# Kernel optimization log

Hardware: AMD Instinct MI355X
Metric: run time of the kernel (lower is better)

The kernel has to match this reference:

```python
import jax, jax.numpy as jnp
import numpy as np

TAU = 2.0        # tau_m
EPS = 1e-5       # BatchNorm eps
SG_GAIN = 4.0    # surrogate gradient gain for LIF nodes
GATE_GAIN = 10.0 # SCALPerceptionLayer gain
GATE_VTH = 0.5   # SCALPerceptionLayer v_th_init


def _spike(v, v_th, gain):
    # Heaviside forward, sigmoid surrogate backward (straight-through).
    s = jax.nn.sigmoid(gain * (v - v_th))
    hard = (v >= v_th).astype(v.dtype)
    return s + jax.lax.stop_gradient(hard - s)


def _lif(x, v_th):
    # single-step LIF, zero initial membrane: v = v0 + (x - v0)/tau = x/tau
    return _spike(x / TAU, v_th, SG_GAIN)


def _bn(x, gamma, beta):
    # BatchNorm1d over channel dim D of (B, N, D): stats over (B, N)
    m = x.mean(axis=(0, 1))
    v = x.var(axis=(0, 1))
    return (x - m) * jax.lax.rsqrt(v + EPS) * gamma + beta


def setup_inputs() -> dict:
    B, N, D, H = 4, 1024, 1024, 16
    key = jax.random.key(0)
    ks = jax.random.split(key, 12)
    def lin(k, out_f, in_f):
        return jax.random.normal(k, (out_f, in_f), jnp.float32) * (in_f ** -0.5)
    inp = {"x": jax.random.normal(ks[0], (B, N, D), jnp.float32)}
    for i, nm in enumerate(["q", "k", "v", "p"]):
        inp[f"W{nm}"] = lin(ks[1 + i], D, D)
        inp[f"b{nm}"] = jnp.zeros((D,), jnp.float32)
        inp[f"g{nm}"] = jnp.ones((D,), jnp.float32)   # BN gamma
        inp[f"beta{nm}"] = jnp.zeros((D,), jnp.float32)  # BN beta
    inp["Wg"] = lin(ks[10], H, D)  # logic_core linear
    inp["bg"] = jnp.zeros((H,), jnp.float32)
    return inp


def reference(x, Wq, bq, gq, betaq, Wk, bk, gk, betak,
              Wv, bv, gv, betav, Wp, bp, gp, betap, Wg, bg):
    B, N, D = x.shape
    H = Wg.shape[0]
    hd = D // H
    scale = hd ** -0.125

    def branch(W, b, g, beta):
        # Linear -> BN (over channels) -> LIF spike -> (B,H,N,hd)
        s = _lif(_bn(x @ W.T + b, g, beta), 1.0)
        return s.reshape(B, N, H, hd).transpose(0, 2, 1, 3)

    q = branch(Wq, bq, gq, betaq)
    k = branch(Wk, bk, gk, betak)
    v = branch(Wv, bv, gv, betav)

    # LogicGateController: energy (B,H) -> repeat to (B,D) -> spiking linear gate
    energy = (q * k).sum(axis=-1).mean(axis=-1)            # (B, H)
    energy_feat = jnp.tile(energy, (1, D // H))            # (B, D)
    gate = _spike(energy_feat @ Wg.T + bg, GATE_VTH, GATE_GAIN)  # (B, H)
    gate = gate[:, :, None, None]                          # (B, H, 1, 1)

    attn = jnp.einsum('bhnd,bhmd->bhnm', q, k) * scale     # (B,H,N,N)
    x_attn = jnp.einsum('bhnm,bhmd->bhnd', attn * gate, v) # (B,H,N,hd)
    x_attn = x_attn.transpose(0, 2, 1, 3).reshape(B, N, D)
    x_attn = _lif(x_attn, 0.5)                             # attn_lif, v_th=0.5

    out = _lif(_bn(x_attn @ Wp.T + bp, gp, betap), 1.0)    # proj path
    return out
```

## Files before the change

### kernel.cpp

```cpp
#include <hip/hip_runtime.h>
#include <cstddef>
#include <cstdint>

#define EPS 1e-5f

typedef __bf16 bf16x8 __attribute__((ext_vector_type(8)));
typedef float f32x4 __attribute__((ext_vector_type(4)));
typedef unsigned short u16x8 __attribute__((ext_vector_type(8)));

__device__ __forceinline__ unsigned short f2bf(float f) {
  unsigned u = __builtin_bit_cast(unsigned, f);
  unsigned r = u + 0x7FFFu + ((u >> 16) & 1u);
  return (unsigned short)(r >> 16);
}
__device__ __forceinline__ float bf2f(unsigned short h) {
  unsigned u = (unsigned)h << 16;
  return __builtin_bit_cast(float, u);
}

__device__ __forceinline__ void gl_lds16(const void* g, void* l) {
  __builtin_amdgcn_global_load_lds(
      (const __attribute__((address_space(1))) unsigned int*)g,
      (__attribute__((address_space(3))) unsigned int*)l, 16, 0, 0);
}

template <int MODE>
__global__ __launch_bounds__(256) void gemm_bf16_bt(
    const unsigned short* __restrict__ A,
    const unsigned short* __restrict__ W0, const unsigned short* __restrict__ W1,
    const float* __restrict__ b0, const float* __restrict__ b1,
    unsigned short* __restrict__ Y, double* __restrict__ psum, double* __restrict__ psq,
    const int* __restrict__ flags, int N, int Kc)
{
  if (MODE == 2) { if (flags[0] == 0) return; }

  __shared__ unsigned short As[2][8192];
  __shared__ unsigned short Bs[2][8192];
  const int tid = threadIdx.x;

  const int bid = blockIdx.x + (blockIdx.y << 3) + (blockIdx.z << 8);
  const int nwg = (int)gridDim.z << 8;
  const int cpx = nwg >> 3;
  const int sw = (bid & 7) * cpx + (bid >> 3);
  const int bx = sw & 7, by = (sw >> 3) & 31, z = sw >> 8;

  const unsigned short* Bm = z ? W1 : W0;
  const float* bias = z ? b1 : b0;
  unsigned short* Yz = Y + (size_t)z * 4096 * N;

  const int bm = by * 128, bn = bx * 128;
  const int lane = tid & 63, w = tid >> 6;
  const int wr = w >> 1, wc = w & 1;
  const int l15 = lane & 15, g = lane >> 4;

  f32x4 acc[4][4] = {};

  bool skip = false;
  if (MODE == 1) skip = (flags[1 + (by >> 3)] == 0);

  if (!skip) {
    const unsigned short* aSrc[4]; const unsigned short* bSrc[4]; int dOff[4];
#pragma unroll
    for (int c = 0; c < 4; ++c) {
      int S = c * 256 + tid;
      int row = S >> 3, sp = S & 7;
      int sl = sp ^ (row & 7);
      aSrc[c] = A  + (size_t)(bm + row) * Kc + sl * 8;
      bSrc[c] = Bm + (size_t)(bn + row) * Kc + sl * 8;
      dOff[c] = S * 8;
    }
    int aOff[4][2], bOff[4][2];
#pragma unroll
    for (int i = 0; i < 4; ++i)
#pragma unroll
      for (int t = 0; t < 2; ++t) {
        int rowA = wr * 64 + i * 16 + l15;
        aOff[i][t] = rowA * 64 + ((t * 4 + g) ^ (rowA & 7)) * 8;
        int rowB = wc * 64 + i * 16 + l15;
        bOff[i][t] = rowB * 64 + ((t * 4 + g) ^ (rowB & 7)) * 8;
      }

    const int nk = Kc >> 6;
#pragma unroll
    for (int c = 0; c < 4; ++c) { gl_lds16(aSrc[c], &As[0][dOff[c]]); aSrc[c] += 64; }
#pragma unroll
    for (int c = 0; c < 4; ++c) { gl_lds16(bSrc[c], &Bs[0][dOff[c]]); bSrc[c] += 64; }
    __syncthreads();

    int cur = 0;
    for (int kt = 0; kt < nk; ++kt) {
      if (kt + 1 < nk) {
#pragma unroll
        for (int c = 0; c < 4; ++c) { gl_lds16(aSrc[c], &As[cur ^ 1][dOff[c]]); aSrc[c] += 64; }
#pragma unroll
        for (int c = 0; c < 4; ++c) { gl_lds16(bSrc[c], &Bs[cur ^ 1][dOff[c]]); bSrc[c] += 64; }
      }
#pragma unroll
      for (int t = 0; t < 2; ++t) {
        bf16x8 af[4], bfr[4];
#pragma unroll
        for (int i = 0; i < 4; ++i) af[i] = *(const bf16x8*)&As[cur][aOff[i][t]];
#pragma unroll
        for (int j = 0; j < 4; ++j) bfr[j] = *(const bf16x8*)&Bs[cur][bOff[j][t]];
#pragma unroll
        for (int i = 0; i < 4; ++i)
#pragma unroll
          for (int j = 0; j < 4; ++j)
            acc[i][j] = __builtin_amdgcn_mfma_f32_16x16x32_bf16(af[i], bfr[j], acc[i][j], 0, 0, 0);
      }
      __syncthreads();
      cur ^= 1;
    }
  }

  const int r0 = bm + wr * 64 + g * 4;
  float csum[4], csq[4];
#pragma unroll
  for (int j = 0; j < 4; ++j) { csum[j] = 0.f; csq[j] = 0.f; }
#pragma unroll
  for (int j = 0; j < 4; ++j) {
    int col = bn + wc * 64 + j * 16 + l15;
    float bv = bias[col];
#pragma unroll
    for (int i = 0; i < 4; ++i)
#pragma unroll
      for (int r = 0; r < 4; ++r) {
        float yv = acc[i][j][r] + bv;
        unsigned short h = f2bf(yv);
        float yb = bf2f(h);
        Yz[(size_t)(r0 + i * 16 + r) * N + col] = h;
        csum[j] += yb;
        csq[j] += yb * yb;
      }
  }
  __syncthreads();
  float* Ls = (float*)&As[0][0];
  const int slot = wr * 4 + g;
#pragma unroll
  for (int j = 0; j < 4; ++j) {
    int ci = wc * 64 + j * 16 + l15;
    Ls[slot * 128 + ci] = csum[j];
    Ls[1024 + slot * 128 + ci] = csq[j];
  }
  __syncthreads();
  if (tid < 128) {
    double s = 0.0, q = 0.0;
#pragma unroll
    for (int sl = 0; sl < 8; ++sl) {
      s += (double)Ls[sl * 128 + tid];
      q += (double)Ls[1024 + sl * 128 + tid];
    }
    size_t o = ((size_t)z * 32 + by) * N + bn + tid;
    psum[o] = s;
    psq[o] = q;
  }
}

__global__ void prep_kernel(const float* __restrict__ x,
                            const float* __restrict__ Wq, const float* __restrict__ Wk,
                            const float* __restrict__ Wv, const float* __restrict__ Wp,
                            unsigned short* __restrict__ Xh, unsigned short* __restrict__ Wh3,
                            unsigned short* __restrict__ Wpcat)
{
  int bid = blockIdx.x, tid = threadIdx.x;
  if (bid < 3584) {
    const float* src; unsigned short* dst; size_t base;
    if (bid < 2048) {
      src = x; dst = Xh; base = ((size_t)bid * 256 + tid) * 8;
    } else {
      int r = bid - 2048, z = r >> 9, blk = r & 511;
      src = (z == 0) ? Wq : ((z == 1) ? Wk : Wv);
      dst = Wh3 + (size_t)z * 1024 * 1024;
      base = ((size_t)blk * 256 + tid) * 8;
    }
    float4 a = *reinterpret_cast<const float4*>(&src[base]);
    float4 b = *reinterpret_cast<const float4*>(&src[base + 4]);
    u16x8 o;
    o[0] = f2bf(a.x); o[1] = f2bf(a.y); o[2] = f2bf(a.z); o[3] = f2bf(a.w);
    o[4] = f2bf(b.x); o[5] = f2bf(b.y); o[6] = f2bf(b.z); o[7] = f2bf(b.w);
    *reinterpret_cast<u16x8*>(&dst[base]) = o;
  } else {
    int blk = bid - 3584;
    size_t base = ((size_t)blk * 256 + tid) * 8;
    int r = (int)(base >> 10), c = (int)(base & 1023);
    float4 a = *reinterpret_cast<const float4*>(&Wp[base]);
    float4 b = *reinterpret_cast<const float4*>(&Wp[base + 4]);
    u16x8 hi, lo;
    hi[0] = f2bf(a.x); lo[0] = f2bf(a.x - bf2f(hi[0]));
    hi[1] = f2bf(a.y); lo[1] = f2bf(a.y - bf2f(hi[1]));
    hi[2] = f2bf(a.z); lo[2] = f2bf(a.z - bf2f(hi[2]));
    hi[3] = f2bf(a.w); lo[3] = f2bf(a.w - bf2f(hi[3]));
    hi[4] = f2bf(b.x); lo[4] = f2bf(b.x - bf2f(hi[4]));
    hi[5] = f2bf(b.y); lo[5] = f2bf(b.y - bf2f(hi[5]));
    hi[6] = f2bf(b.z); lo[6] = f2bf(b.z - bf2f(hi[6]));
    hi[7] = f2bf(b.w); lo[7] = f2bf(b.w - bf2f(hi[7]));
    unsigned short* Or = Wpcat + (size_t)r * 2048;
    *reinterpret_cast<u16x8*>(&Or[c]) = hi;
    *reinterpret_cast<u16x8*>(&Or[1024 + c]) = lo;
  }
}

__global__ void bn_finalize(const double* __restrict__ psum, const double* __restrict__ psq,
                            const float* __restrict__ g0, const float* __restrict__ g1,
                            float* __restrict__ meanv, float* __restrict__ Av,
                            const int* __restrict__ runflag,
                            int* __restrict__ zflags, int* __restrict__ zenergy,
                            int N, double invM)
{
  if (zflags && blockIdx.x == 0 && blockIdx.y == 0) {
    int t = threadIdx.x;
    if (t < 5) zflags[t] = 0;
    if (t >= 64 && t < 128) zenergy[t - 64] = 0;
  }
  if (runflag && runflag[0] == 0) return;
  int z = blockIdx.y;
  const float* g = z ? g1 : g0;
  int c = blockIdx.x * blockDim.x + threadIdx.x;
  double s = 0.0, q = 0.0;
  for (int rb = 0; rb < 32; ++rb) {
    s += psum[((size_t)z * 32 + rb) * N + c];
    q += psq [((size_t)z * 32 + rb) * N + c];
  }
  double m = s * invM;
  double var = q * invM - m * m;
  if (var < 0.0) var = 0.0;
  meanv[(size_t)z * N + c] = (float)m;
  Av[(size_t)z * N + c] = g[(size_t)c] * rsqrtf((float)var + EPS);
}

__global__ void spike_qk_energy(const unsigned short* __restrict__ Yq,
                                const unsigned short* __restrict__ Yk,
                                const float* __restrict__ meanv, const float* __restrict__ Av,
                                const float* __restrict__ beq, const float* __restrict__ bek,
                                unsigned short* __restrict__ qb, unsigned short* __restrict__ kb,
                                int* __restrict__ energy_int, int N)
{
  const int tid = threadIdx.x;
  const int c0 = (tid * 8) & (N - 1);
  const int head = c0 >> 6;
  const int batch = blockIdx.x >> 7;
  const float* mq = meanv;            const float* aq = Av;
  const float* mk = meanv + N;        const float* ak = Av + N;
  __shared__ int bins[16];
  if (tid < 16) bins[tid] = 0;
  __syncthreads();
  int cnt = 0;
#pragma unroll
  for (int j = 0; j < 4; ++j) {
    size_t base = (size_t)blockIdx.x * 8192 + j * 2048 + tid * 8;
    u16x8 yq = *reinterpret_cast<const u16x8*>(&Yq[base]);
    u16x8 yk = *reinterpret_cast<const u16x8*>(&Yk[base]);
    u16x8 oq, ok;
#pragma unroll
    for (int e = 0; e < 8; ++e) {
      bool sq = (bf2f(yq[e]) - mq[c0 + e]) * aq[c0 + e] + beq[c0 + e] >= 2.0f;
      bool sk = (bf2f(yk[e]) - mk[c0 + e]) * ak[c0 + e] + bek[c0 + e] >= 2.0f;
      oq[e] = sq ? 0x3F80 : 0;
      ok[e] = sk ? 0x3F80 : 0;
      cnt += (sq && sk) ? 1 : 0;
    }
    *reinterpret_cast<u16x8*>(&qb[base]) = oq;
    *reinterpret_cast<u16x8*>(&kb[base]) = ok;
  }
  atomicAdd(&bins[head], cnt);
  __syncthreads();
  if (tid < 16) atomicAdd(&energy_int[batch * 16 + tid], bins[tid]);
}

__global__ void spike_v(const unsigned short* __restrict__ Yv,
                        const float* __restrict__ meanv, const float* __restrict__ Av,
                        const float* __restrict__ beta, unsigned short* __restrict__ vb,
                        const int* __restrict__ flags, int N)
{
  if (flags[0] == 0) return;
  size_t base = ((size_t)blockIdx.x * 256 + threadIdx.x) * 8;
  int c0 = (int)(base & (size_t)(N - 1));
  u16x8 y8 = *reinterpret_cast<const u16x8*>(&Yv[base]);
  u16x8 o;
#pragma unroll
  for (int e = 0; e < 8; ++e)
    o[e] = ((bf2f(y8[e]) - meanv[c0 + e]) * Av[c0 + e] + beta[c0 + e] >= 2.0f) ? 0x3F80 : 0;
  *reinterpret_cast<u16x8*>(&vb[base]) = o;
}

__global__ void bn_spike_f32(const unsigned short* __restrict__ Y,
                             const float* __restrict__ meanv, const float* __restrict__ Av,
                             const float* __restrict__ beta, float* __restrict__ S, int N)
{
  size_t base = ((size_t)blockIdx.x * 256 + threadIdx.x) * 8;
  int c0 = (int)(base & (size_t)(N - 1));
  u16x8 y8 = *reinterpret_cast<const u16x8*>(&Y[base]);
  float4 o0, o1;
  o0.x = ((bf2f(y8[0]) - meanv[c0 + 0]) * Av[c0 + 0] + beta[c0 + 0] >= 2.0f) ? 1.f : 0.f;
  o0.y = ((bf2f(y8[1]) - meanv[c0 + 1]) * Av[c0 + 1] + beta[c0 + 1] >= 2.0f) ? 1.f : 0.f;
  o0.z = ((bf2f(y8[2]) - meanv[c0 + 2]) * Av[c0 + 2] + beta[c0 + 2] >= 2.0f) ? 1.f : 0.f;
  o0.w = ((bf2f(y8[3]) - meanv[c0 + 3]) * Av[c0 + 3] + beta[c0 + 3] >= 2.0f) ? 1.f : 0.f;
  o1.x = ((bf2f(y8[4]) - meanv[c0 + 4]) * Av[c0 + 4] + beta[c0 + 4] >= 2.0f) ? 1.f : 0.f;
  o1.y = ((bf2f(y8[5]) - meanv[c0 + 5]) * Av[c0 + 5] + beta[c0 + 5] >= 2.0f) ? 1.f : 0.f;
  o1.z = ((bf2f(y8[6]) - meanv[c0 + 6]) * Av[c0 + 6] + beta[c0 + 6] >= 2.0f) ? 1.f : 0.f;
  o1.w = ((bf2f(y8[7]) - meanv[c0 + 7]) * Av[c0 + 7] + beta[c0 + 7] >= 2.0f) ? 1.f : 0.f;
  *reinterpret_cast<float4*>(&S[base]) = o0;
  *reinterpret_cast<float4*>(&S[base + 4]) = o1;
}

__global__ void gate_kernel(const int* __restrict__ energy_int, const float* __restrict__ Wg,
                            const float* __restrict__ bg, float* __restrict__ gate,
                            int* __restrict__ flags, int D)
{
  int b = blockIdx.x >> 4, hp = blockIdx.x & 15;
  int tid = threadIdx.x;
  float e[16];
#pragma unroll
  for (int h = 0; h < 16; ++h) e[h] = (float)energy_int[b * 16 + h] * (1.f / 1024.f);
  float s = 0.f;
  for (int j = tid; j < D; j += 256) s = fmaf(e[j & 15], Wg[(size_t)hp * D + j], s);
  __shared__ float red[256];
  red[tid] = s;
  __syncthreads();
  for (int off = 128; off; off >>= 1) {
    if (tid < off) red[tid] += red[tid + off];
    __syncthreads();
  }
  if (tid == 0) {
    int gv = (red[0] + bg[hp] >= 0.5f) ? 1 : 0;
    gate[blockIdx.x] = (float)gv;
    if (gv) { atomicOr(&flags[0], 1); atomicOr(&flags[1 + b], 1); }
  }
}

__global__ __launch_bounds__(256) void attn_kernel(
    const unsigned short* __restrict__ qb, const unsigned short* __restrict__ kb,
    const unsigned short* __restrict__ vb, const float* __restrict__ gate,
    const int* __restrict__ flags, unsigned short* __restrict__ xs,
    int Ntok, int D, float scale)
{
  int bh = blockIdx.x;
  int b = bh >> 4, h = bh & 15;
  if (flags[1 + b] == 0) return;
  int n0 = blockIdx.y * 32;
  int tid = threadIdx.x;
  unsigned short* outbase = xs + (size_t)(b * Ntok + n0) * 2048 + h * 64;

  if (gate[bh] == 0.f) {
    ushort4 zv = {0, 0, 0, 0};
    for (int i = tid; i < 32 * 16; i += 256) {
      int r = i >> 4, c4 = (i & 15) << 2;
      *reinterpret_cast<ushort4*>(&outbase[(size_t)r * 2048 + c4]) = zv;
      *reinterpret_cast<ushort4*>(&outbase[(size_t)r * 2048 + 1024 + c4]) = zv;
    }
    return;
  }

  __shared__ float qs[32][68], ks[32][68], vs[32][68], Ss[32][36];
  const unsigned short* qg = qb + (size_t)b * Ntok * D + h * 64;
  const unsigned short* kg = kb + (size_t)b * Ntok * D + h * 64;
  const unsigned short* vg = vb + (size_t)b * Ntok * D + h * 64;

  {
    int r = tid >> 3, c8 = (tid & 7) * 8;
    u16x8 t = *reinterpret_cast<const u16x8*>(&qg[(size_t)(n0 + r) * D + c8]);
#pragma unroll
    for (int e = 0; e < 8; ++e) qs[r][c8 + e] = bf2f(t[e]);
  }

  float acc[8];
#pragma unroll
  for (int j = 0; j < 8; ++j) acc[j] = 0.f;
  const int nloc = tid >> 3;
  const int dd0 = (tid & 7) * 8;

  for (int mt = 0; mt < Ntok / 32; ++mt) {
    int m0 = mt * 32;
    __syncthreads();
    {
      int r = tid >> 3, c8 = (tid & 7) * 8;
      u16x8 tk = *reinterpret_cast<const u16x8*>(&kg[(size_t)(m0 + r) * D + c8]);
      u16x8 tv = *reinterpret_cast<const u16x8*>(&vg[(size_t)(m0 + r) * D + c8]);
#pragma unroll
      for (int e = 0; e < 8; ++e) { ks[r][c8 + e] = bf2f(tk[e]); vs[r][c8 + e] = bf2f(tv[e]); }
    }
    __syncthreads();
    {
      int np = tid >> 3;
      int mp0 = (tid & 7) * 4;
      float s0 = 0.f, s1 = 0.f, s2 = 0.f, s3 = 0.f;
#pragma unroll 8
      for (int d = 0; d < 64; ++d) {
        float qv = qs[np][d];
        s0 = fmaf(qv, ks[mp0 + 0][d], s0);
        s1 = fmaf(qv, ks[mp0 + 1][d], s1);
        s2 = fmaf(qv, ks[mp0 + 2][d], s2);
        s3 = fmaf(qv, ks[mp0 + 3][d], s3);
      }
      Ss[np][mp0 + 0] = s0; Ss[np][mp0 + 1] = s1;
      Ss[np][mp0 + 2] = s2; Ss[np][mp0 + 3] = s3;
    }
    __syncthreads();
#pragma unroll 8
    for (int mp = 0; mp < 32; ++mp) {
      float sv = Ss[nloc][mp];
#pragma unroll
      for (int j = 0; j < 8; ++j) acc[j] = fmaf(sv, vs[mp][dd0 + j], acc[j]);
    }
  }

#pragma unroll
  for (int j = 0; j < 8; ++j) {
    float x = scale * acc[j];
    unsigned short sp = (x >= 1.0f) ? 0x3F80 : 0;
    outbase[(size_t)nloc * 2048 + dd0 + j] = sp;
    outbase[(size_t)nloc * 2048 + 1024 + dd0 + j] = sp;
  }
}

extern "C" void kernel_launch(void* const* d_in, const int* in_sizes, int n_in,
                              void* d_out, int out_size, void* d_ws, size_t ws_size,
                              hipStream_t stream)
{
  (void)in_sizes; (void)n_in; (void)out_size; (void)ws_size;
  const int Ntok = 1024, D = 1024;
  const int M = 4096;
  const float scale = 0.5946035575013605f;

  const float* x     = (const float*)d_in[0];
  const float* Wq    = (const float*)d_in[1];
  const float* bq    = (const float*)d_in[2];
  const float* gq    = (const float*)d_in[3];
  const float* betaq = (const float*)d_in[4];
  const float* Wk    = (const float*)d_in[5];
  const float* bk    = (const float*)d_in[6];
  const float* gk    = (const float*)d_in[7];
  const float* betak = (const float*)d_in[8];
  const float* Wv    = (const float*)d_in[9];
  const float* bv    = (const float*)d_in[10];
  const float* gv    = (const float*)d_in[11];
  const float* betav = (const float*)d_in[12];
  const float* Wp    = (const float*)d_in[13];
  const float* bp    = (const float*)d_in[14];
  const float* gp    = (const float*)d_in[15];
  const float* betap = (const float*)d_in[16];
  const float* Wg    = (const float*)d_in[17];
  const float* bg    = (const float*)d_in[18];

  char* w = (char*)d_ws;
  const size_t MB = 1024 * 1024;
  const size_t MN = (size_t)M * D;
  unsigned short* Y3bf  = (unsigned short*)(w + 0 * MB);
  unsigned short* xat2  = (unsigned short*)(w + 0 * MB);
  unsigned short* Yv    = Y3bf + 2 * MN;
  unsigned short* Yp    = (unsigned short*)(w + 24 * MB);
  unsigned short* Wpcat = (unsigned short*)(w + 32 * MB);
  unsigned short* Xh    = (unsigned short*)(w + 48 * MB);
  unsigned short* Wh3   = (unsigned short*)(w + 56 * MB);
  unsigned short* qb2   = (unsigned short*)(w + 62 * MB);
  unsigned short* kb2   = (unsigned short*)(w + 70 * MB);
  unsigned short* vb2   = (unsigned short*)(w + 78 * MB);
  double* psum   = (double*)(w + 86 * MB);
  double* psq    = (double*)(w + 87 * MB);
  float*  meanv  = (float*)(w + 88 * MB);
  float*  Av     = (float*)(w + 88 * MB + 16384);
  int*    energy_int = (int*)(w + 88 * MB + 32768);
  int*    flags  = (int*)(w + 88 * MB + 32768 + 512);
  float*  gate   = (float*)(w + 88 * MB + 32768 + 1024);

  float* out = (float*)d_out;
  unsigned short* Whq = Wh3;
  unsigned short* Whk = Wh3 + MN / 4;
  unsigned short* Whv = Wh3 + MN / 2;

  prep_kernel<<<dim3(4096), 256, 0, stream>>>(x, Wq, Wk, Wv, Wp, Xh, Wh3, Wpcat);

  gemm_bf16_bt<0><<<dim3(8, 32, 2), 256, 0, stream>>>(
      Xh, Whq, Whk, bq, bk, Y3bf, psum, psq, nullptr, D, 1024);
  bn_finalize<<<dim3(4, 2), 256, 0, stream>>>(
      psum, psq, gq, gk, meanv, Av, nullptr, flags, energy_int, D, 1.0 / M);
  spike_qk_energy<<<dim3(512), 256, 0, stream>>>(
      Y3bf, Y3bf + MN, meanv, Av, betaq, betak, qb2, kb2, energy_int, D);

  gate_kernel<<<dim3(64), 256, 0, stream>>>(energy_int, Wg, bg, gate, flags, D);

  gemm_bf16_bt<2><<<dim3(8, 32, 1), 256, 0, stream>>>(
      Xh, Whv, Whv, bv, bv, Yv, psum + 2 * 32 * (size_t)D, psq + 2 * 32 * (size_t)D,
      flags, D, 1024);
  bn_finalize<<<dim3(4, 1), 256, 0, stream>>>(
      psum + 2 * 32 * (size_t)D, psq + 2 * 32 * (size_t)D, gv, gv,
      meanv + 2 * D, Av + 2 * D, flags, nullptr, nullptr, D, 1.0 / M);
  spike_v<<<dim3(2048), 256, 0, stream>>>(Yv, meanv + 2 * D, Av + 2 * D, betav, vb2, flags, D);

  attn_kernel<<<dim3(64, Ntok / 32), 256, 0, stream>>>(
      qb2, kb2, vb2, gate, flags, xat2, Ntok, D, scale);

  gemm_bf16_bt<1><<<dim3(8, 32, 1), 256, 0, stream>>>(
      xat2, Wpcat, Wpcat, bp, bp, Yp, psum, psq, flags, D, 2048);
  bn_finalize<<<dim3(4, 1), 256, 0, stream>>>(
      psum, psq, gp, gp, meanv, Av, nullptr, nullptr, nullptr, D, 1.0 / M);
  bn_spike_f32<<<dim3(2048), 256, 0, stream>>>(Yp, meanv, Av, betap, out, D);
}
```

Baseline: 78.99 us.

## Split weight prep by gate flag, relax GEMM LDS waits, unroll BN finalize

The combined prep kernel is split so that only x, Wq and Wk are converted before the first GEMM. Wv and the hi/lo split of Wp are now converted after the gate kernel, and that step is skipped entirely when the gate flag says the attention path is inactive. In the GEMM K-loop, the blanket __syncthreads is replaced by explicit vmcnt waits plus raw s_barrier, so the next tile's global-to-LDS loads can stay in flight while the current tile is consumed. The BN finalize reduction is unrolled with two accumulators. The hand-written waitcnt assumes eight outstanding loads per thread, which is fragile if the compiler reorders or adds memory operations.

```diff
diff --git a/kernel.cpp b/kernel.cpp
--- a/kernel.cpp
+++ b/kernel.cpp
@@ -85,7 +85,6 @@
     for (int c = 0; c < 4; ++c) { gl_lds16(aSrc[c], &As[0][dOff[c]]); aSrc[c] += 64; }
 #pragma unroll
     for (int c = 0; c < 4; ++c) { gl_lds16(bSrc[c], &Bs[0][dOff[c]]); bSrc[c] += 64; }
-    __syncthreads();
 
     int cur = 0;
     for (int kt = 0; kt < nk; ++kt) {
@@ -94,21 +93,30 @@
         for (int c = 0; c < 4; ++c) { gl_lds16(aSrc[c], &As[cur ^ 1][dOff[c]]); aSrc[c] += 64; }
 #pragma unroll
         for (int c = 0; c < 4; ++c) { gl_lds16(bSrc[c], &Bs[cur ^ 1][dOff[c]]); bSrc[c] += 64; }
+        asm volatile("s_waitcnt vmcnt(8)" ::: "memory");
+      } else {
+        asm volatile("s_waitcnt vmcnt(0)" ::: "memory");
       }
-#pragma unroll
-      for (int t = 0; t < 2; ++t) {
-        bf16x8 af[4], bfr[4];
-#pragma unroll
-        for (int i = 0; i < 4; ++i) af[i] = *(const bf16x8*)&As[cur][aOff[i][t]];
-#pragma unroll
-        for (int j = 0; j < 4; ++j) bfr[j] = *(const bf16x8*)&Bs[cur][bOff[j][t]];
-#pragma unroll
-        for (int i = 0; i < 4; ++i)
-#pragma unroll
-          for (int j = 0; j < 4; ++j)
-            acc[i][j] = __builtin_amdgcn_mfma_f32_16x16x32_bf16(af[i], bfr[j], acc[i][j], 0, 0, 0);
+      __builtin_amdgcn_s_barrier();
+      __builtin_amdgcn_sched_barrier(0);
+      {
+        const unsigned short* Ac = &As[cur][0];
+        const unsigned short* Bc = &Bs[cur][0];
+#pragma unroll
+        for (int t = 0; t < 2; ++t) {
+          bf16x8 af[4], bfr[4];
+#pragma unroll
+          for (int i = 0; i < 4; ++i) af[i] = *(const bf16x8*)&Ac[aOff[i][t]];
+#pragma unroll
+          for (int j = 0; j < 4; ++j) bfr[j] = *(const bf16x8*)&Bc[bOff[j][t]];
+#pragma unroll
+          for (int i = 0; i < 4; ++i)
+#pragma unroll
+            for (int j = 0; j < 4; ++j)
+              acc[i][j] = __builtin_amdgcn_mfma_f32_16x16x32_bf16(af[i], bfr[j], acc[i][j], 0, 0, 0);
+        }
       }
-      __syncthreads();
+      __builtin_amdgcn_s_barrier();
       cur ^= 1;
     }
   }
@@ -156,32 +164,43 @@
   }
 }
 
-__global__ void prep_kernel(const float* __restrict__ x,
-                            const float* __restrict__ Wq, const float* __restrict__ Wk,
-                            const float* __restrict__ Wv, const float* __restrict__ Wp,
-                            unsigned short* __restrict__ Xh, unsigned short* __restrict__ Wh3,
-                            unsigned short* __restrict__ Wpcat)
+__global__ void prep1_kernel(const float* __restrict__ x,
+                             const float* __restrict__ Wq, const float* __restrict__ Wk,
+                             unsigned short* __restrict__ Xh, unsigned short* __restrict__ Wh3)
 {
   int bid = blockIdx.x, tid = threadIdx.x;
-  if (bid < 3584) {
-    const float* src; unsigned short* dst; size_t base;
-    if (bid < 2048) {
-      src = x; dst = Xh; base = ((size_t)bid * 256 + tid) * 8;
-    } else {
-      int r = bid - 2048, z = r >> 9, blk = r & 511;
-      src = (z == 0) ? Wq : ((z == 1) ? Wk : Wv);
-      dst = Wh3 + (size_t)z * 1024 * 1024;
-      base = ((size_t)blk * 256 + tid) * 8;
-    }
-    float4 a = *reinterpret_cast<const float4*>(&src[base]);
-    float4 b = *reinterpret_cast<const float4*>(&src[base + 4]);
+  const float* src; unsigned short* dst; size_t base;
+  if (bid < 2048) {
+    src = x; dst = Xh; base = ((size_t)bid * 256 + tid) * 8;
+  } else if (bid < 2560) {
+    src = Wq; dst = Wh3; base = ((size_t)(bid - 2048) * 256 + tid) * 8;
+  } else {
+    src = Wk; dst = Wh3 + (size_t)1024 * 1024; base = ((size_t)(bid - 2560) * 256 + tid) * 8;
+  }
+  float4 a = *reinterpret_cast<const float4*>(&src[base]);
+  float4 b = *reinterpret_cast<const float4*>(&src[base + 4]);
+  u16x8 o;
+  o[0] = f2bf(a.x); o[1] = f2bf(a.y); o[2] = f2bf(a.z); o[3] = f2bf(a.w);
+  o[4] = f2bf(b.x); o[5] = f2bf(b.y); o[6] = f2bf(b.z); o[7] = f2bf(b.w);
+  *reinterpret_cast<u16x8*>(&dst[base]) = o;
+}
+
+__global__ void prep2_kernel(const float* __restrict__ Wv, const float* __restrict__ Wp,
+                             unsigned short* __restrict__ Whv, unsigned short* __restrict__ Wpcat,
+                             const int* __restrict__ flags)
+{
+  if (flags[0] == 0) return;
+  int bid = blockIdx.x, tid = threadIdx.x;
+  if (bid < 512) {
+    size_t base = ((size_t)bid * 256 + tid) * 8;
+    float4 a = *reinterpret_cast<const float4*>(&Wv[base]);
+    float4 b = *reinterpret_cast<const float4*>(&Wv[base + 4]);
     u16x8 o;
     o[0] = f2bf(a.x); o[1] = f2bf(a.y); o[2] = f2bf(a.z); o[3] = f2bf(a.w);
     o[4] = f2bf(b.x); o[5] = f2bf(b.y); o[6] = f2bf(b.z); o[7] = f2bf(b.w);
-    *reinterpret_cast<u16x8*>(&dst[base]) = o;
+    *reinterpret_cast<u16x8*>(&Whv[base]) = o;
   } else {
-    int blk = bid - 3584;
-    size_t base = ((size_t)blk * 256 + tid) * 8;
+    size_t base = ((size_t)(bid - 512) * 256 + tid) * 8;
     int r = (int)(base >> 10), c = (int)(base & 1023);
     float4 a = *reinterpret_cast<const float4*>(&Wp[base]);
     float4 b = *reinterpret_cast<const float4*>(&Wp[base + 4]);
@@ -216,11 +235,15 @@
   int z = blockIdx.y;
   const float* g = z ? g1 : g0;
   int c = blockIdx.x * blockDim.x + threadIdx.x;
-  double s = 0.0, q = 0.0;
-  for (int rb = 0; rb < 32; ++rb) {
-    s += psum[((size_t)z * 32 + rb) * N + c];
-    q += psq [((size_t)z * 32 + rb) * N + c];
-  }
+  const double* ps = psum + (size_t)z * 32 * N + c;
+  const double* pq = psq  + (size_t)z * 32 * N + c;
+  double s0 = 0, s1 = 0, q0 = 0, q1 = 0;
+#pragma unroll
+  for (int rb = 0; rb < 32; rb += 2) {
+    s0 += ps[(size_t)rb * N];       q0 += pq[(size_t)rb * N];
+    s1 += ps[(size_t)(rb + 1) * N]; q1 += pq[(size_t)(rb + 1) * N];
+  }
+  double s = s0 + s1, q = q0 + q1;
   double m = s * invM;
   double var = q * invM - m * m;
   if (var < 0.0) var = 0.0;
@@ -468,7 +491,7 @@
   unsigned short* Whk = Wh3 + MN / 4;
   unsigned short* Whv = Wh3 + MN / 2;
 
-  prep_kernel<<<dim3(4096), 256, 0, stream>>>(x, Wq, Wk, Wv, Wp, Xh, Wh3, Wpcat);
+  prep1_kernel<<<dim3(3072), 256, 0, stream>>>(x, Wq, Wk, Xh, Wh3);
 
   gemm_bf16_bt<0><<<dim3(8, 32, 2), 256, 0, stream>>>(
       Xh, Whq, Whk, bq, bk, Y3bf, psum, psq, nullptr, D, 1024);
@@ -478,6 +501,8 @@
       Y3bf, Y3bf + MN, meanv, Av, betaq, betak, qb2, kb2, energy_int, D);
 
   gate_kernel<<<dim3(64), 256, 0, stream>>>(energy_int, Wg, bg, gate, flags, D);
+
+  prep2_kernel<<<dim3(1024), 256, 0, stream>>>(Wv, Wp, Whv, Wpcat, flags);
 
   gemm_bf16_bt<2><<<dim3(8, 32, 1), 256, 0, stream>>>(
       Xh, Whv, Whv, bv, bv, Yv, psum + 2 * 32 * (size_t)D, psq + 2 * 32 * (size_t)D,
```

Result: faster. 75.63 us (median of 2 runs) (-4.3%).
